# Kernel tuning notes

Hardware: AMD Instinct MI355X
Metric: run time of the kernel (lower is better)

## Reference

```python
import jax, jax.numpy as jnp
import numpy as np

H = 128  # GRU hidden dim

def gru_sequence(x_emb, W_ih, W_hh, b_ih, b_hh):
    """Run a GRU over x_emb (S, B, E); return final-step output (B, H).
    Matches torch.nn.GRU gate math:
      r = sig(W_ir x + b_ir + W_hr h + b_hr)
      z = sig(W_iz x + b_iz + W_hz h + b_hz)
      n = tanh(W_in x + b_in + r * (W_hn h + b_hn))
      h' = (1 - z) * n + z * h
    """
    S, B, E = x_emb.shape
    # Precompute input projections for all timesteps: (S, B, 3H)
    gx_all = jnp.einsum('sbe,ge->sbg', x_emb, W_ih) + b_ih

    def step(h, gx):
        gh = h @ W_hh.T + b_hh               # (B, 3H)
        r = jax.nn.sigmoid(gx[:, :H] + gh[:, :H])
        z = jax.nn.sigmoid(gx[:, H:2*H] + gh[:, H:2*H])
        n = jnp.tanh(gx[:, 2*H:] + r * gh[:, 2*H:])
        h_new = (1.0 - z) * n + z * h
        return h_new, None

    h0 = jnp.zeros((B, H), dtype=x_emb.dtype)
    h_final, _ = jax.lax.scan(step, h0, gx_all)
    return h_final  # (B, H) == out at last timestep


def setup_inputs() -> dict:
    key = jax.random.key(0)
    ks = jax.random.split(key, 12)
    S, B, V, E = 512, 512, 50000, 50
    x1 = jax.random.randint(ks[0], (S, B), 0, V, dtype=jnp.int32)
    x2 = jax.random.randint(ks[1], (S, B), 0, V, dtype=jnp.int32)
    emb = jax.random.uniform(ks[2], (V, E), jnp.float32, -0.01, 0.01)
    s = 1.0 / np.sqrt(H)
    W_ih = jax.random.uniform(ks[3], (3*H, E), jnp.float32, -s, s)
    W_hh = jax.random.uniform(ks[4], (3*H, H), jnp.float32, -s, s)
    b_ih = jax.random.uniform(ks[5], (3*H,), jnp.float32, -s, s)
    b_hh = jax.random.uniform(ks[6], (3*H,), jnp.float32, -s, s)
    s1 = 1.0 / np.sqrt(2*H)
    W1 = jax.random.uniform(ks[7], (H, 2*H), jnp.float32, -s1, s1)
    b1 = jax.random.uniform(ks[8], (H,), jnp.float32, -s1, s1)
    s2 = 1.0 / np.sqrt(H)
    W2 = jax.random.uniform(ks[9], (1, H), jnp.float32, -s2, s2)
    b2 = jax.random.uniform(ks[10], (1,), jnp.float32, -s2, s2)
    return {"x1": x1, "x2": x2, "emb": emb, "W_ih": W_ih, "W_hh": W_hh,
            "b_ih": b_ih, "b_hh": b_hh, "W1": W1, "b1": b1, "W2": W2, "b2": b2}


def reference(x1, x2, emb, W_ih, W_hh, b_ih, b_hh, W1, b1, W2, b2):
    e1 = emb[x1]  # (S, B, E)
    e2 = emb[x2]
    h1 = gru_sequence(e1, W_ih, W_hh, b_ih, b_hh)  # (B, H)
    h2 = gru_sequence(e2, W_ih, W_hh, b_ih, b_hh)  # (B, H)
    fc_in = jnp.concatenate([h1, h2], axis=-1)     # (B, 2H)
    hid = jax.nn.relu(fc_in @ W1.T + b1)
    out = jax.nn.sigmoid(hid @ W2.T + b2)          # (B, 1)
    return out
```

## Files before the change

### kernel.cpp

```cpp
#include <hip/hip_runtime.h>
#include <hip/hip_bf16.h>
#include <stdint.h>

#define S_LEN 512
#define BATCH 512
#define HID   128
#define G3    384
#define EMB   50
#define VOC   50000

#define NL2E  (-1.4426950408889634f)
#define N2L2E (-2.8853900817779268f)

typedef __attribute__((ext_vector_type(8))) short short8;
typedef __attribute__((ext_vector_type(4))) float float4v;

__device__ inline unsigned short f2bf(float f) {
  union { float f; uint32_t u; } v; v.f = f;
  uint32_t u = v.u;
  u += 0x7fffu + ((u >> 16) & 1u);
  return (unsigned short)(u >> 16);
}
__device__ inline float bf2f(unsigned short h) {
  union { uint32_t u; float f; } v; v.u = ((uint32_t)h) << 16;
  return v.f;
}
__device__ inline uint32_t fbits(float f) {
  union { float f; uint32_t u; } v; v.f = f; return v.u;
}
__device__ inline float fast_sig(float x) {
  return __builtin_amdgcn_rcpf(1.f + __expf(-x));
}

__device__ inline short8 load8_bf_padded(const float* __restrict__ row, int k0,
                                         float sc) {
  float f[8];
  if (k0 + 7 < EMB) {
    float4v a = *(const float4v*)(row + k0);
    float4v b = *(const float4v*)(row + k0 + 4);
#pragma unroll
    for (int i = 0; i < 4; ++i) { f[i] = a[i]; f[i + 4] = b[i]; }
  } else {
#pragma unroll
    for (int i = 0; i < 8; ++i) f[i] = (k0 + i < EMB) ? row[k0 + i] : 0.f;
  }
  short8 s;
#pragma unroll
  for (int i = 0; i < 8; ++i) s[i] = (short)f2bf(f[i] * sc);
  return s;
}

__global__ __launch_bounds__(256) void build_gxv(
    const float* __restrict__ emb, const float* __restrict__ W_ih,
    const float* __restrict__ b_ih, const float* __restrict__ b_hh,
    unsigned short* __restrict__ gxv) {
  __shared__ __align__(16) unsigned short cmat[64][392];
  const int w  = threadIdx.x >> 6;
  const int L  = threadIdx.x & 63;
  const int q  = L >> 4;
  const int ln = L & 15;
  const int vbase = blockIdx.x * 64 + w * 16;
  const int vloc  = w * 16;

  const int vr = min(vbase + ln, VOC - 1);
  const float* arow = emb + (size_t)vr * EMB;
  short8 afr0 = load8_bf_padded(arow, q * 8, 1.f);
  short8 afr1 = load8_bf_padded(arow, 32 + q * 8, 1.f);

  int gg = ln;
  float sc = NL2E;
  short8 b0 = load8_bf_padded(W_ih + (size_t)gg * EMB, q * 8, sc);
  short8 b1 = load8_bf_padded(W_ih + (size_t)gg * EMB, 32 + q * 8, sc);
  float bias = sc * (b_ih[gg] + b_hh[gg]);

  for (int nt = 0; nt < 24; ++nt) {
    short8 nb0, nb1; float nbias;
    if (nt < 23) {
      const int g2 = (nt + 1) * 16 + ln;
      const float s2 = (g2 < 256) ? NL2E : N2L2E;
      const float* brow = W_ih + (size_t)g2 * EMB;
      nb0 = load8_bf_padded(brow, q * 8, s2);
      nb1 = load8_bf_padded(brow, 32 + q * 8, s2);
      nbias = s2 * (b_ih[g2] + (g2 < 256 ? b_hh[g2] : 0.f));
    }
    float4v acc = {bias, bias, bias, bias};
    acc = __builtin_amdgcn_mfma_f32_16x16x32_bf16(afr0, b0, acc, 0, 0, 0);
    acc = __builtin_amdgcn_mfma_f32_16x16x32_bf16(afr1, b1, acc, 0, 0, 0);
#pragma unroll
    for (int r = 0; r < 4; ++r)
      cmat[vloc + q * 4 + r][gg] = f2bf(acc[r]);
    gg += 16; b0 = nb0; b1 = nb1; bias = nbias;
  }
  __syncthreads();

  for (int idx = threadIdx.x; idx < 3072; idx += 256) {
    const int row = idx / 48, c8 = idx - row * 48;
    const int vrow = blockIdx.x * 64 + row;
    if (vrow < VOC) {
      short8 v = *(const short8*)(&cmat[row][c8 * 8]);
      *(short8*)(gxv + (size_t)vrow * G3 + c8 * 8) = v;
    }
  }
}

__global__ __launch_bounds__(512) void gru_kernel(
    const int* __restrict__ x1, const int* __restrict__ x2,
    const unsigned short* __restrict__ gxv, const float* __restrict__ W_hh,
    const float* __restrict__ b_hh, float* __restrict__ fcin) {
  const int bid   = blockIdx.x;
  const int gru   = bid >> 7;
  const int chunk = bid & 127;
  const int* xs   = gru ? x2 : x1;

  const int tid = threadIdx.x;
  const int w  = tid >> 6;
  const int L  = tid & 63;
  const int q  = L >> 4;
  const int ln = L & 15;
  const int jb = w * 16;
  const int jl = L >> 2, n = L & 3;
  const int j  = jb + jl;
  const int ng = chunk * 4 + n;

  __shared__ __align__(16) unsigned short hbuf[2][512];
  __shared__ __align__(16) float scr[3][4][136];

  short8 afrag[3][4];
#pragma unroll
  for (int t = 0; t < 3; ++t) {
    const float sc = (t < 2) ? NL2E : N2L2E;
    const float* wr = W_hh + (size_t)(t * 128 + jb + ln) * HID;
#pragma unroll
    for (int kf = 0; kf < 4; ++kf) {
      const int k0 = kf * 32 + q * 8;
      float4v f0 = *(const float4v*)(wr + k0);
      float4v f1 = *(const float4v*)(wr + k0 + 4);
      short8 a;
#pragma unroll
      for (int i = 0; i < 4; ++i) a[i] = (short)f2bf(f0[i] * sc);
#pragma unroll
      for (int i = 0; i < 4; ++i) a[i + 4] = (short)f2bf(f1[i] * sc);
      afrag[t][kf] = a;
    }
  }

  float4v bhn4;
#pragma unroll
  for (int r = 0; r < 4; ++r) bhn4[r] = N2L2E * b_hh[2 * 128 + jb + q * 4 + r];

  for (int idx = tid; idx < 1024; idx += 512) ((unsigned short*)hbuf)[idx] = 0;

  float h = 0.f;

  const int tok0 = xs[ng];
  unsigned short gxr, gxz, gxnn;
  {
    const unsigned short* gp = gxv + (size_t)tok0 * G3;
    gxr = gp[j]; gxz = gp[128 + j]; gxnn = gp[256 + j];
  }
  int tok1 = xs[BATCH + ng];

  const int wofs = (((j >> 3) * 4 + n) << 3) + (j & 7);
  const int rofs = ((q * 4 + (ln & 3)) << 3);

  __syncthreads();

  for (int s = 0; s < S_LEN; ++s) {
    unsigned short pr, pz, pn;
    {
      const unsigned short* gp = gxv + (size_t)tok1 * G3;
      pr = gp[j]; pz = gp[128 + j]; pn = gp[256 + j];
    }
    const int s2 = (s + 2 < S_LEN) ? (s + 2) : 0;
    const int tok2 = xs[s2 * BATCH + ng];

    const unsigned short* rb = hbuf[s & 1];
    short8 bfrag[4];
#pragma unroll
    for (int kf = 0; kf < 4; ++kf)
      bfrag[kf] = *(const short8*)(rb + kf * 128 + rofs);

    float4v acc[3];
#pragma unroll
    for (int t = 0; t < 3; ++t) {
      float4v a0 = (t == 2) ? bhn4 : (float4v){0.f, 0.f, 0.f, 0.f};
      float4v a1 = {0.f, 0.f, 0.f, 0.f};
      a0 = __builtin_amdgcn_mfma_f32_16x16x32_bf16(afrag[t][0], bfrag[0], a0, 0, 0, 0);
      a1 = __builtin_amdgcn_mfma_f32_16x16x32_bf16(afrag[t][1], bfrag[1], a1, 0, 0, 0);
      a0 = __builtin_amdgcn_mfma_f32_16x16x32_bf16(afrag[t][2], bfrag[2], a0, 0, 0, 0);
      a1 = __builtin_amdgcn_mfma_f32_16x16x32_bf16(afrag[t][3], bfrag[3], a1, 0, 0, 0);
      acc[t] = a0 + a1;
    }

    if (ln < 4) {
#pragma unroll
      for (int t = 0; t < 3; ++t)
        *(float4v*)(&scr[t][ln][jb + q * 4]) = acc[t];
    }
    const float aR = scr[0][n][j];
    const float aZ = scr[1][n][j];
    const float aN = scr[2][n][j];

    const float gr = bf2f(gxr) + aR;
    const float gz = bf2f(gxz) + aZ;
    const float rg = __builtin_amdgcn_rcpf(1.f + __builtin_amdgcn_exp2f(gr));
    const float zg = __builtin_amdgcn_rcpf(1.f + __builtin_amdgcn_exp2f(gz));
    const float pre = bf2f(gxnn) + rg * aN;
    const float sg  = __builtin_amdgcn_rcpf(1.f + __builtin_amdgcn_exp2f(pre));
    const float nn  = 2.f * sg - 1.f;
    h = zg * (h - nn) + nn;

    hbuf[(s + 1) & 1][wofs] = (unsigned short)((fbits(h) + 0x8000u) >> 16);

    asm volatile("s_waitcnt lgkmcnt(0)\n\ts_barrier" ::: "memory");

    gxr = pr; gxz = pz; gxnn = pn;
    tok1 = tok2;
  }

  fcin[(size_t)ng * 256 + gru * 128 + j] = h;
}

__global__ __launch_bounds__(128) void head_kernel(
    const float* __restrict__ fcin, const float* __restrict__ W1,
    const float* __restrict__ b1, const float* __restrict__ W2,
    const float* __restrict__ b2, float* __restrict__ out) {
  __shared__ float fc[256];
  __shared__ float part[2];
  const int b = blockIdx.x, t = threadIdx.x;
  fc[t]       = fcin[(size_t)b * 256 + t];
  fc[t + 128] = fcin[(size_t)b * 256 + t + 128];
  __syncthreads();

  float acc = b1[t];
#pragma unroll 8
  for (int k = 0; k < 256; ++k) acc += W1[t * 256 + k] * fc[k];
  const float hid = fmaxf(acc, 0.f);

  float v = hid * W2[t];
#pragma unroll
  for (int o = 32; o > 0; o >>= 1) v += __shfl_xor(v, o, 64);
  if ((t & 63) == 0) part[t >> 6] = v;
  __syncthreads();
  if (t == 0) {
    const float s = part[0] + part[1] + b2[0];
    out[b] = fast_sig(s);
  }
}

extern "C" void kernel_launch(void* const* d_in, const int* in_sizes, int n_in,
                              void* d_out, int out_size, void* d_ws, size_t ws_size,
                              hipStream_t stream) {
  const int*   x1   = (const int*)d_in[0];
  const int*   x2   = (const int*)d_in[1];
  const float* emb  = (const float*)d_in[2];
  const float* W_ih = (const float*)d_in[3];
  const float* W_hh = (const float*)d_in[4];
  const float* b_ih = (const float*)d_in[5];
  const float* b_hh = (const float*)d_in[6];
  const float* W1   = (const float*)d_in[7];
  const float* b1   = (const float*)d_in[8];
  const float* W2   = (const float*)d_in[9];
  const float* b2   = (const float*)d_in[10];
  float* out = (float*)d_out;

  unsigned short* gxv = (unsigned short*)d_ws;
  float* fcin = (float*)((char*)d_ws + (size_t)VOC * G3 * 2);

  build_gxv<<<(VOC + 63) / 64, 256, 0, stream>>>(emb, W_ih, b_ih, b_hh, gxv);
  gru_kernel<<<256, 512, 0, stream>>>(x1, x2, gxv, W_hh, b_hh, fcin);
  head_kernel<<<512, 128, 0, stream>>>(fcin, W1, b1, W2, b2, out);
}
```

Before: 407.0 us.

## Pre-pack W_ih fragments, remap GRU lanes to drop LDS scratch, prefetch three steps

Adds a small prep kernel that converts W_ih to scaled bf16 MFMA fragments and fused biases once, so build_gxv loads ready fragments instead of converting per block. In the GRU kernel the lane-to-(hidden, batch) mapping now matches the MFMA output layout, so each lane picks its gate value from its own accumulator registers rather than going through an LDS scratch exchange. The gather of input-projection values is prefetched three steps ahead instead of two. The aim is a shorter per-step serial critical path, at the cost of an extra tiny kernel launch and more live registers.

```diff
diff --git a/kernel.cpp b/kernel.cpp
--- a/kernel.cpp
+++ b/kernel.cpp
@@ -32,28 +32,34 @@
   return __builtin_amdgcn_rcpf(1.f + __expf(-x));
 }
 
-__device__ inline short8 load8_bf_padded(const float* __restrict__ row, int k0,
-                                         float sc) {
-  float f[8];
-  if (k0 + 7 < EMB) {
-    float4v a = *(const float4v*)(row + k0);
-    float4v b = *(const float4v*)(row + k0 + 4);
-#pragma unroll
-    for (int i = 0; i < 4; ++i) { f[i] = a[i]; f[i + 4] = b[i]; }
-  } else {
-#pragma unroll
-    for (int i = 0; i < 8; ++i) f[i] = (k0 + i < EMB) ? row[k0 + i] : 0.f;
-  }
-  short8 s;
-#pragma unroll
-  for (int i = 0; i < 8; ++i) s[i] = (short)f2bf(f[i] * sc);
-  return s;
+__global__ __launch_bounds__(128) void prep_wih(
+    const float* __restrict__ W_ih, const float* __restrict__ b_ih,
+    const float* __restrict__ b_hh, unsigned short* __restrict__ wbf,
+    float* __restrict__ sbias) {
+  const int nt = blockIdx.x;
+  const int kf = threadIdx.x >> 6;
+  const int L  = threadIdx.x & 63;
+  const int q = L >> 4, ln = L & 15;
+  const int g = nt * 16 + ln;
+  const float sc = (g < 256) ? NL2E : N2L2E;
+  const int k0 = kf * 32 + q * 8;
+  short8 v;
+#pragma unroll
+  for (int i = 0; i < 8; ++i) {
+    const int k = k0 + i;
+    v[i] = (k < EMB) ? (short)f2bf(W_ih[(size_t)g * EMB + k] * sc) : (short)0;
+  }
+  *(short8*)(wbf + (size_t)((nt * 2 + kf) * 64 + L) * 8) = v;
+  if (threadIdx.x < 16) {
+    const int gg = nt * 16 + threadIdx.x;
+    const float s2 = (gg < 256) ? NL2E : N2L2E;
+    sbias[gg] = s2 * (b_ih[gg] + (gg < 256 ? b_hh[gg] : 0.f));
+  }
 }
 
 __global__ __launch_bounds__(256) void build_gxv(
-    const float* __restrict__ emb, const float* __restrict__ W_ih,
-    const float* __restrict__ b_ih, const float* __restrict__ b_hh,
-    unsigned short* __restrict__ gxv) {
+    const float* __restrict__ emb, const unsigned short* __restrict__ wbf,
+    const float* __restrict__ sbias, unsigned short* __restrict__ gxv) {
   __shared__ __align__(16) unsigned short cmat[64][392];
   const int w  = threadIdx.x >> 6;
   const int L  = threadIdx.x & 63;
@@ -64,32 +70,36 @@
 
   const int vr = min(vbase + ln, VOC - 1);
   const float* arow = emb + (size_t)vr * EMB;
-  short8 afr0 = load8_bf_padded(arow, q * 8, 1.f);
-  short8 afr1 = load8_bf_padded(arow, 32 + q * 8, 1.f);
-
-  int gg = ln;
-  float sc = NL2E;
-  short8 b0 = load8_bf_padded(W_ih + (size_t)gg * EMB, q * 8, sc);
-  short8 b1 = load8_bf_padded(W_ih + (size_t)gg * EMB, 32 + q * 8, sc);
-  float bias = sc * (b_ih[gg] + b_hh[gg]);
+  float fa[16];
+#pragma unroll
+  for (int i = 0; i < 16; ++i) {
+    const int k = ((i < 8) ? q * 8 : 32 + q * 8 - 8) + i;
+    fa[i] = 0.f;
+  }
+  short8 afr0, afr1;
+  {
+    float f[8];
+#pragma unroll
+    for (int i = 0; i < 8; ++i) { const int k = q * 8 + i; f[i] = (k < EMB) ? arow[k] : 0.f; }
+#pragma unroll
+    for (int i = 0; i < 8; ++i) afr0[i] = (short)f2bf(f[i]);
+#pragma unroll
+    for (int i = 0; i < 8; ++i) { const int k = 32 + q * 8 + i; f[i] = (k < EMB) ? arow[k] : 0.f; }
+#pragma unroll
+    for (int i = 0; i < 8; ++i) afr1[i] = (short)f2bf(f[i]);
+  }
 
   for (int nt = 0; nt < 24; ++nt) {
-    short8 nb0, nb1; float nbias;
-    if (nt < 23) {
-      const int g2 = (nt + 1) * 16 + ln;
-      const float s2 = (g2 < 256) ? NL2E : N2L2E;
-      const float* brow = W_ih + (size_t)g2 * EMB;
-      nb0 = load8_bf_padded(brow, q * 8, s2);
-      nb1 = load8_bf_padded(brow, 32 + q * 8, s2);
-      nbias = s2 * (b_ih[g2] + (g2 < 256 ? b_hh[g2] : 0.f));
-    }
+    const short8 b0 = *(const short8*)(wbf + (size_t)((nt * 2 + 0) * 64 + L) * 8);
+    const short8 b1 = *(const short8*)(wbf + (size_t)((nt * 2 + 1) * 64 + L) * 8);
+    const int gg = nt * 16 + ln;
+    const float bias = sbias[gg];
     float4v acc = {bias, bias, bias, bias};
     acc = __builtin_amdgcn_mfma_f32_16x16x32_bf16(afr0, b0, acc, 0, 0, 0);
     acc = __builtin_amdgcn_mfma_f32_16x16x32_bf16(afr1, b1, acc, 0, 0, 0);
 #pragma unroll
     for (int r = 0; r < 4; ++r)
       cmat[vloc + q * 4 + r][gg] = f2bf(acc[r]);
-    gg += 16; b0 = nb0; b1 = nb1; bias = nbias;
   }
   __syncthreads();
 
@@ -118,12 +128,12 @@
   const int q  = L >> 4;
   const int ln = L & 15;
   const int jb = w * 16;
-  const int jl = L >> 2, n = L & 3;
-  const int j  = jb + jl;
+  const int g3 = ln >> 2;
+  const int n  = ln & 3;
+  const int j  = jb + q * 4 + g3;
   const int ng = chunk * 4 + n;
 
   __shared__ __align__(16) unsigned short hbuf[2][512];
-  __shared__ __align__(16) float scr[3][4][136];
 
   short8 afrag[3][4];
 #pragma unroll
@@ -152,27 +162,31 @@
 
   float h = 0.f;
 
-  const int tok0 = xs[ng];
-  unsigned short gxr, gxz, gxnn;
+  unsigned short gxr, gxz, gxnn, nr, nz, nn2;
   {
-    const unsigned short* gp = gxv + (size_t)tok0 * G3;
+    const unsigned short* gp = gxv + (size_t)xs[ng] * G3;
     gxr = gp[j]; gxz = gp[128 + j]; gxnn = gp[256 + j];
-  }
-  int tok1 = xs[BATCH + ng];
+    const unsigned short* gq = gxv + (size_t)xs[BATCH + ng] * G3;
+    nr = gq[j]; nz = gq[128 + j]; nn2 = gq[256 + j];
+  }
+  int tokf = xs[2 * BATCH + ng];
 
   const int wofs = (((j >> 3) * 4 + n) << 3) + (j & 7);
-  const int rofs = ((q * 4 + (ln & 3)) << 3);
+  const int rofs = ((q * 4 + n) << 3);
+
+  const bool selA = (ln & 4) != 0;
+  const bool selB = (ln & 8) != 0;
 
   __syncthreads();
 
   for (int s = 0; s < S_LEN; ++s) {
-    unsigned short pr, pz, pn;
+    unsigned short fr, fz, fn;
     {
-      const unsigned short* gp = gxv + (size_t)tok1 * G3;
-      pr = gp[j]; pz = gp[128 + j]; pn = gp[256 + j];
-    }
-    const int s2 = (s + 2 < S_LEN) ? (s + 2) : 0;
-    const int tok2 = xs[s2 * BATCH + ng];
+      const unsigned short* gp = gxv + (size_t)tokf * G3;
+      fr = gp[j]; fz = gp[128 + j]; fn = gp[256 + j];
+    }
+    const int s3 = (s + 3 < S_LEN) ? (s + 3) : 0;
+    const int tok3 = xs[s3 * BATCH + ng];
 
     const unsigned short* rb = hbuf[s & 1];
     short8 bfrag[4];
@@ -180,7 +194,7 @@
     for (int kf = 0; kf < 4; ++kf)
       bfrag[kf] = *(const short8*)(rb + kf * 128 + rofs);
 
-    float4v acc[3];
+    float vsel[3];
 #pragma unroll
     for (int t = 0; t < 3; ++t) {
       float4v a0 = (t == 2) ? bhn4 : (float4v){0.f, 0.f, 0.f, 0.f};
@@ -189,23 +203,17 @@
       a1 = __builtin_amdgcn_mfma_f32_16x16x32_bf16(afrag[t][1], bfrag[1], a1, 0, 0, 0);
       a0 = __builtin_amdgcn_mfma_f32_16x16x32_bf16(afrag[t][2], bfrag[2], a0, 0, 0, 0);
       a1 = __builtin_amdgcn_mfma_f32_16x16x32_bf16(afrag[t][3], bfrag[3], a1, 0, 0, 0);
-      acc[t] = a0 + a1;
-    }
-
-    if (ln < 4) {
-#pragma unroll
-      for (int t = 0; t < 3; ++t)
-        *(float4v*)(&scr[t][ln][jb + q * 4]) = acc[t];
-    }
-    const float aR = scr[0][n][j];
-    const float aZ = scr[1][n][j];
-    const float aN = scr[2][n][j];
-
-    const float gr = bf2f(gxr) + aR;
-    const float gz = bf2f(gxz) + aZ;
+      const float4v acc = a0 + a1;
+      const float x0 = selA ? acc[1] : acc[0];
+      const float x1 = selA ? acc[3] : acc[2];
+      vsel[t] = selB ? x1 : x0;
+    }
+
+    const float gr = bf2f(gxr) + vsel[0];
+    const float gz = bf2f(gxz) + vsel[1];
     const float rg = __builtin_amdgcn_rcpf(1.f + __builtin_amdgcn_exp2f(gr));
     const float zg = __builtin_amdgcn_rcpf(1.f + __builtin_amdgcn_exp2f(gz));
-    const float pre = bf2f(gxnn) + rg * aN;
+    const float pre = bf2f(gxnn) + rg * vsel[2];
     const float sg  = __builtin_amdgcn_rcpf(1.f + __builtin_amdgcn_exp2f(pre));
     const float nn  = 2.f * sg - 1.f;
     h = zg * (h - nn) + nn;
@@ -214,8 +222,9 @@
 
     asm volatile("s_waitcnt lgkmcnt(0)\n\ts_barrier" ::: "memory");
 
-    gxr = pr; gxz = pz; gxnn = pn;
-    tok1 = tok2;
+    gxr = nr; gxz = nz; gxnn = nn2;
+    nr = fr; nz = fz; nn2 = fn;
+    tokf = tok3;
   }
 
   fcin[(size_t)ng * 256 + gru * 128 + j] = h;
@@ -264,10 +273,14 @@
   const float* b2   = (const float*)d_in[10];
   float* out = (float*)d_out;
 
-  unsigned short* gxv = (unsigned short*)d_ws;
-  float* fcin = (float*)((char*)d_ws + (size_t)VOC * G3 * 2);
-
-  build_gxv<<<(VOC + 63) / 64, 256, 0, stream>>>(emb, W_ih, b_ih, b_hh, gxv);
+  char* ws = (char*)d_ws;
+  unsigned short* gxv = (unsigned short*)ws;
+  float* fcin = (float*)(ws + (size_t)VOC * G3 * 2);
+  unsigned short* wbf = (unsigned short*)(ws + (size_t)VOC * G3 * 2 + 524288);
+  float* sbias = (float*)(ws + (size_t)VOC * G3 * 2 + 524288 + 49152);
+
+  prep_wih<<<24, 128, 0, stream>>>(W_ih, b_ih, b_hh, wbf, sbias);
+  build_gxv<<<(VOC + 63) / 64, 256, 0, stream>>>(emb, wbf, sbias, gxv);
   gru_kernel<<<256, 512, 0, stream>>>(x1, x2, gxv, W_hh, b_hh, fcin);
   head_kernel<<<512, 128, 0, stream>>>(fcin, W1, b1, W2, b2, out);
 }
```

Measured after the change: 346.7 us. -14.8%, faster.
